# Kernel optimization log

Hardware: AMD Instinct MI355X
Metric: run time of the kernel (lower is better)

The kernel has to match this reference:

```python
import jax, jax.numpy as jnp
import numpy as np

K = 7          # kernel_size
STRIDE = 1
GC = 4         # group_channels (fixed in module)
BN_EPS = 1e-5


def setup_inputs() -> dict:
    key = jax.random.key(0)
    ks = jax.random.split(key, 4)
    B, C, H, W = 4, 256, 56, 56
    Cr = C // 4              # reduction_ratio = 4
    G = C // GC              # groups = 64
    K2 = K * K               # 49
    x = jax.random.normal(ks[0], (B, C, H, W), jnp.float32)
    w1 = jax.random.normal(ks[1], (Cr, C), jnp.float32) * 0.05   # conv1 1x1
    b1 = jnp.zeros((Cr,), jnp.float32)
    gamma = jnp.ones((Cr,), jnp.float32)
    beta = jnp.zeros((Cr,), jnp.float32)
    bn_mean = jnp.zeros((Cr,), jnp.float32)
    bn_var = jnp.ones((Cr,), jnp.float32)
    w2 = jax.random.normal(ks[2], (K2 * G, Cr), jnp.float32) * 0.05  # conv2 1x1
    b2 = jnp.zeros((K2 * G,), jnp.float32)
    return {"x": x, "w1": w1, "b1": b1, "gamma": gamma, "beta": beta,
            "bn_mean": bn_mean, "bn_var": bn_var, "w2": w2, "b2": b2}


def reference(x, w1, b1, gamma, beta, bn_mean, bn_var, w2, b2):
    B, C, H, W = x.shape
    G = C // GC
    K2 = K * K
    p = (K - 1) // 2

    # kernel-generation branch (stride == 1 -> no avgpool)
    y = jnp.einsum('oc,bchw->bohw', w1, x) + b1[None, :, None, None]
    # BatchNorm (inference, running stats)
    inv = gamma / jnp.sqrt(bn_var + BN_EPS)
    y = y * inv[None, :, None, None] + (beta - bn_mean * inv)[None, :, None, None]
    y = jax.nn.relu(y)
    weight = jnp.einsum('oc,bchw->bohw', w2, y) + b2[None, :, None, None]
    Ho, Wo = weight.shape[2], weight.shape[3]
    weight = weight.reshape(B, G, K2, Ho, Wo)

    # unfold: zero-pad then gather k*k shifted views (channel-major like torch Unfold)
    xp = jnp.pad(x, ((0, 0), (0, 0), (p, p), (p, p)))
    patches = jnp.stack(
        [xp[:, :, i:i + H:STRIDE, j:j + W:STRIDE] for i in range(K) for j in range(K)],
        axis=2)                                    # (B, C, K2, Ho, Wo)
    patches = patches.reshape(B, G, GC, K2, Ho, Wo)

    # per-pixel dynamic kernel multiply-accumulate over k^2
    out = jnp.einsum('bgkhw,bgckhw->bgchw', weight, patches)
    return out.reshape(B, C, Ho, Wo)
```

## Files before the change

### kernel.cpp

```cpp
#include <hip/hip_runtime.h>
#include <hip/hip_fp16.h>

typedef _Float16 h8 __attribute__((ext_vector_type(8)));
typedef _Float16 h2v __attribute__((ext_vector_type(2)));
typedef __fp16 fp16x2 __attribute__((ext_vector_type(2)));
typedef float f32x4 __attribute__((ext_vector_type(4)));

#define HW 3136
#define NPX 12544
#define YSTR 96
#define XROW 14
#define XSEG 148
#define PS2 456
#define WGT32_W 7296

union UH { unsigned int u; h2v h; fp16x2 p; };
__device__ __forceinline__ h2v uh(unsigned int u) { UH v; v.u = u; return v.h; }
__device__ __forceinline__ unsigned int hu(h2v h) { UH v; v.h = h; return v.u; }
#define BLO(w) __builtin_shufflevector(w, w, 0, 0)
#define BHI(w) __builtin_shufflevector(w, w, 1, 1)

__device__ __forceinline__ unsigned int pkrtz(float a, float b) {
    UH v; v.p = __builtin_amdgcn_cvt_pkrtz(a, b); return v.u;
}
__device__ __forceinline__ unsigned short f2hu(float f) {
    union { __half h; unsigned short u; } v; v.h = __float2half(f); return v.u;
}
__device__ __forceinline__ float fget(const float4& v, int e) {
    return e == 0 ? v.x : e == 1 ? v.y : e == 2 ? v.z : v.w;
}

__global__ __launch_bounds__(256) void kyw(
    const float* __restrict__ x, const float* __restrict__ w1,
    const float* __restrict__ b1, const float* __restrict__ gamma,
    const float* __restrict__ beta, const float* __restrict__ mean,
    const float* __restrict__ var, const float* __restrict__ w2,
    const float* __restrict__ b2, unsigned short* __restrict__ ytb,
    unsigned short* __restrict__ w2b96)
{
    __shared__ unsigned short xt[64 * 264];
    const int t = threadIdx.x, bid = blockIdx.x;

    if (bid >= 196) {
        const int r0 = (bid - 196) * 16;
#pragma unroll
        for (int i = 0; i < 6; ++i) {
            int j = i * 256 + t;
            int row = r0 + j / 96, col = j - (j / 96) * 96;
            int c8 = row / 448, rem = row - c8 * 448;
            int g = rem / 56, s = rem - g * 56;
            int ki = s >> 3, kj = s & 7;
            float v = 0.f;
            if (kj < 7) {
                int o = (c8 * 8 + g) * 49 + ki * 7 + kj;
                v = col < 64 ? w2[o * 64 + col] : (col == 64 ? b2[o] : 0.f);
            }
            w2b96[row * 96 + col] = f2hu(v);
        }
        return;
    }

    const int px0 = bid * 64;
    const int b = px0 / HW;
    const int p0 = px0 - b * HW;

    {
        unsigned int* xw = (unsigned int*)xt;
#pragma unroll
        for (int s = 0; s < 4; ++s)
#pragma unroll
            for (int i = 0; i < 2; ++i) {
                int j = i * 256 + t;
                int cp2 = j >> 2, pq = j & 3;
                const float* s0 = x + (size_t)(b * 256 + cp2 * 2) * HW
                                    + p0 + s * 16 + pq * 4;
                float4 v0 = *(const float4*)(s0);
                float4 v1 = *(const float4*)(s0 + HW);
                int pxb = s * 16 + pq * 4;
                xw[(pxb + 0) * 132 + cp2] = pkrtz(v0.x, v1.x);
                xw[(pxb + 1) * 132 + cp2] = pkrtz(v0.y, v1.y);
                xw[(pxb + 2) * 132 + cp2] = pkrtz(v0.z, v1.z);
                xw[(pxb + 3) * 132 + cp2] = pkrtz(v0.w, v1.w);
            }
    }
    if (t < 64) {
        unsigned short* yr = ytb + (size_t)(px0 + t) * YSTR + 64;
        ushort4 one; one.x = 0x3C00u; one.y = 0; one.z = 0; one.w = 0;
        ushort4 z; z.x = 0; z.y = 0; z.z = 0; z.w = 0;
        *(ushort4*)(yr) = one;
#pragma unroll
        for (int q = 1; q < 8; ++q) *(ushort4*)(yr + q * 4) = z;
    }
    __syncthreads();

    const int lane = t & 63, wave = t >> 6;
    const int n = lane & 15, quad = lane >> 4;
    const int m0 = wave * 16;

    h8 A[8];
#pragma unroll
    for (int k = 0; k < 8; ++k) {
        const float* wrow = w1 + (m0 + n) * 256 + k * 32 + quad * 8;
        float4 wa = *(const float4*)(wrow);
        float4 wb = *(const float4*)(wrow + 4);
        union { uint4 u; h8 h; } Au;
        Au.u.x = pkrtz(wa.x, wa.y);
        Au.u.y = pkrtz(wa.z, wa.w);
        Au.u.z = pkrtz(wb.x, wb.y);
        Au.u.w = pkrtz(wb.z, wb.w);
        A[k] = Au.h;
    }
    float sc[4], sh[4];
#pragma unroll
    for (int r = 0; r < 4; ++r) {
        int m = m0 + quad * 4 + r;
        sc[r] = gamma[m] * rsqrtf(var[m] + 1e-5f);
        sh[r] = beta[m] - mean[m] * sc[r] + b1[m] * sc[r];
    }

#pragma unroll
    for (int s = 0; s < 4; ++s) {
        f32x4 acc = {0.f, 0.f, 0.f, 0.f};
#pragma unroll
        for (int k = 0; k < 8; ++k) {
            h8 bv = *(const h8*)(&xt[(s * 16 + n) * 264 + k * 32 + quad * 8]);
            acc = __builtin_amdgcn_mfma_f32_16x16x32_f16(A[k], bv, acc, 0, 0, 0);
        }
        uint2 pk;
        pk.x = pkrtz(fmaxf(acc[0] * sc[0] + sh[0], 0.f),
                     fmaxf(acc[1] * sc[1] + sh[1], 0.f));
        pk.y = pkrtz(fmaxf(acc[2] * sc[2] + sh[2], 0.f),
                     fmaxf(acc[3] * sc[3] + sh[3], 0.f));
        *(uint2*)(ytb + (size_t)(px0 + s * 16 + n) * YSTR + m0 + quad * 4) = pk;
    }
}

__global__ __launch_bounds__(256, 4) void kmain(
    const float* __restrict__ x, const unsigned short* __restrict__ w2b96,
    const unsigned short* __restrict__ ytb, float* __restrict__ out)
{
    __shared__ __align__(16) unsigned int smem_u[WGT32_W + 16 * XSEG];
    unsigned short* wgt16 = (unsigned short*)smem_u;
    unsigned int* xsb = smem_u + WGT32_W;

    const int t = threadIdx.x;
    const int pix = t & 15, sub = t >> 4;
    const int lane = t & 63, wave = t >> 6;
    const int bc = blockIdx.x;
    const int b = bc >> 3, c8 = bc & 7;
    const int w0 = blockIdx.y * 8, h0 = blockIdx.z * 4;
    const int ph = pix >> 3, pw = pix & 7;
    const int n = lane & 15, quad = lane >> 4;

    h8 bfa[3], bfb[3];
    {
        const int Pa = b * HW + (h0 + (n >> 3)) * 56 + w0 + (n & 7);
        const unsigned short* ya = ytb + (size_t)Pa * YSTR + quad * 8;
        bfa[0] = *(const h8*)(ya);
        bfa[1] = *(const h8*)(ya + 32);
        bfa[2] = *(const h8*)(ya + 64);
        const unsigned short* yb = ya + (size_t)112 * YSTR;
        bfb[0] = *(const h8*)(yb);
        bfb[1] = *(const h8*)(yb + 32);
        bfb[2] = *(const h8*)(yb + 64);
    }

    if (t < 160) {
        const int seg = t & 15, jr = t >> 4;
        const int jg = seg >> 1, jcp = seg & 1;
        const int hh = h0 + jr - 3;
        const bool rowok = (hh >= 0) && (hh < 56);
        const float* src = x + ((size_t)b * 256 + c8 * 32 + jg * 4 + jcp * 2) * HW + hh * 56;
        float4 va[2][4];
#pragma unroll
        for (int q = 0; q < 4; ++q) {
            int col0 = w0 - 4 + q * 4;
            bool ok = rowok && (col0 >= 0) && (col0 <= 52);
#pragma unroll
            for (int ci = 0; ci < 2; ++ci)
                va[ci][q] = ok ? *(const float4*)(src + ci * HW + col0)
                              : make_float4(0.f, 0.f, 0.f, 0.f);
        }
        unsigned int* dst = xsb + seg * XSEG + jr * XROW;
#pragma unroll
        for (int q = 0; q < 4; ++q)
#pragma unroll
            for (int e = 0; e < 4; ++e) {
                int c = q * 4 + e - 1;
                if (c >= 0 && c < 14)
                    dst[c] = pkrtz(fget(va[0][q], e), fget(va[1][q], e));
            }
    }

    {
        const int c0 = c8 * 448;
        for (int tile = wave; tile < 28; tile += 4) {
            const unsigned short* ap = w2b96 + (size_t)(c0 + tile * 16 + n) * 96 + quad * 8;
            h8 af0 = *(const h8*)(ap);
            h8 af1 = *(const h8*)(ap + 32);
            h8 af2 = *(const h8*)(ap + 64);
            f32x4 aca = {0.f, 0.f, 0.f, 0.f};
            aca = __builtin_amdgcn_mfma_f32_16x16x32_f16(af0, bfa[0], aca, 0, 0, 0);
            aca = __builtin_amdgcn_mfma_f32_16x16x32_f16(af1, bfa[1], aca, 0, 0, 0);
            aca = __builtin_amdgcn_mfma_f32_16x16x32_f16(af2, bfa[2], aca, 0, 0, 0);
            f32x4 acb = {0.f, 0.f, 0.f, 0.f};
            acb = __builtin_amdgcn_mfma_f32_16x16x32_f16(af0, bfb[0], acb, 0, 0, 0);
            acb = __builtin_amdgcn_mfma_f32_16x16x32_f16(af1, bfb[1], acb, 0, 0, 0);
            acb = __builtin_amdgcn_mfma_f32_16x16x32_f16(af2, bfb[2], acb, 0, 0, 0);
            uint2 pka, pkb;
            pka.x = pkrtz(aca[0], aca[1]);
            pka.y = pkrtz(aca[2], aca[3]);
            pkb.x = pkrtz(acb[0], acb[1]);
            pkb.y = pkrtz(acb[2], acb[3]);
            *(uint2*)(wgt16 + n * PS2 + tile * 16 + quad * 4) = pka;
            *(uint2*)(wgt16 + (16 + n) * PS2 + tile * 16 + quad * 4) = pkb;
        }
    }
    __syncthreads();

    const int g = sub & 7, cp = sub >> 3;
    const unsigned int* xrb = xsb + (g * 2 + cp) * XSEG + pw;
#pragma unroll
    for (int php = 0; php < 2; ++php) {
        const unsigned short* wr16 = wgt16 + (php * 16 + pix) * PS2 + g * 56;
        const unsigned int* xr = xrb + (php * 2 + ph) * XROW;
        h2v acA = {(_Float16)0.f, (_Float16)0.f};
        h2v acB = acA;
#pragma unroll
        for (int ki = 0; ki < 7; ++ki) {
            uint4 wq = *(const uint4*)(wr16 + ki * 8);
            const unsigned int* xrow = xr + ki * XROW;
            unsigned int xv[7];
#pragma unroll
            for (int j = 0; j < 7; ++j) xv[j] = xrow[j];
            h2v w01 = uh(wq.x), w23 = uh(wq.y), w45 = uh(wq.z), w6p = uh(wq.w);
            acA += BLO(w01) * uh(xv[0]);
            acB += BHI(w01) * uh(xv[1]);
            acA += BLO(w23) * uh(xv[2]);
            acB += BHI(w23) * uh(xv[3]);
            acA += BLO(w45) * uh(xv[4]);
            acB += BHI(w45) * uh(xv[5]);
            acA += BLO(w6p) * uh(xv[6]);
        }
        h2v acc2 = acA + acB;
        int h = h0 + php * 2 + ph;
        size_t ob = ((size_t)b * 256 + c8 * 32 + g * 4 + cp * 2) * HW + h * 56 + w0 + pw;
        out[ob] = (float)acc2[0];
        out[ob + HW] = (float)acc2[1];
    }
}

extern "C" void kernel_launch(void* const* d_in, const int* in_sizes, int n_in,
                              void* d_out, int out_size, void* d_ws, size_t ws_size,
                              hipStream_t stream) {
    const float* x     = (const float*)d_in[0];
    const float* w1    = (const float*)d_in[1];
    const float* b1    = (const float*)d_in[2];
    const float* gamma = (const float*)d_in[3];
    const float* beta  = (const float*)d_in[4];
    const float* mean  = (const float*)d_in[5];
    const float* var   = (const float*)d_in[6];
    const float* w2    = (const float*)d_in[7];
    const float* b2    = (const float*)d_in[8];
    float* out = (float*)d_out;

    unsigned short* ytb   = (unsigned short*)d_ws;
    unsigned short* w2b96 = ytb + (size_t)NPX * YSTR;
    hipLaunchKernelGGL(kyw, dim3(420), dim3(256), 0, stream,
                       x, w1, b1, gamma, beta, mean, var, w2, b2, ytb, w2b96);
    hipLaunchKernelGGL(kmain, dim3(32, 7, 14), dim3(256), 0, stream,
                       x, w2b96, ytb, out);
}
```

Baseline: 121.7 us.

## Halve LDS weight buffer by staging second pixel half in registers

The per-pixel dynamic weights for the second 16-pixel half are held in registers (7 packed uint2 per thread) rather than written to shared memory alongside the first half. The LDS weight region is halved and reused: the first half is consumed, then the buffer is overwritten with the second half between two extra barriers. This lowers LDS per block so that six blocks per CU can be resident (launch bounds raised from 4 to 6). In exchange it adds two __syncthreads and extra register pressure from the held values.

```diff
diff --git a/kernel.cpp b/kernel.cpp
--- a/kernel.cpp
+++ b/kernel.cpp
@@ -12,7 +12,7 @@
 #define XROW 14
 #define XSEG 148
 #define PS2 456
-#define WGT32_W 7296
+#define WGT_W 3648
 
 union UH { unsigned int u; h2v h; fp16x2 p; };
 __device__ __forceinline__ h2v uh(unsigned int u) { UH v; v.u = u; return v.h; }
@@ -135,13 +135,13 @@
     }
 }
 
-__global__ __launch_bounds__(256, 4) void kmain(
+__global__ __launch_bounds__(256, 6) void kmain(
     const float* __restrict__ x, const unsigned short* __restrict__ w2b96,
     const unsigned short* __restrict__ ytb, float* __restrict__ out)
 {
-    __shared__ __align__(16) unsigned int smem_u[WGT32_W + 16 * XSEG];
+    __shared__ __align__(16) unsigned int smem_u[WGT_W + 16 * XSEG];
     unsigned short* wgt16 = (unsigned short*)smem_u;
-    unsigned int* xsb = smem_u + WGT32_W;
+    unsigned int* xsb = smem_u + WGT_W;
 
     const int t = threadIdx.x;
     const int pix = t & 15, sub = t >> 4;
@@ -159,10 +159,10 @@
         bfa[0] = *(const h8*)(ya);
         bfa[1] = *(const h8*)(ya + 32);
         bfa[2] = *(const h8*)(ya + 64);
-        const unsigned short* yb = ya + (size_t)112 * YSTR;
-        bfb[0] = *(const h8*)(yb);
-        bfb[1] = *(const h8*)(yb + 32);
-        bfb[2] = *(const h8*)(yb + 64);
+        const unsigned short* yb2 = ya + (size_t)112 * YSTR;
+        bfb[0] = *(const h8*)(yb2);
+        bfb[1] = *(const h8*)(yb2 + 32);
+        bfb[2] = *(const h8*)(yb2 + 64);
     }
 
     if (t < 160) {
@@ -192,9 +192,12 @@
             }
     }
 
+    uint2 pkb[7];
     {
         const int c0 = c8 * 448;
-        for (int tile = wave; tile < 28; tile += 4) {
+#pragma unroll
+        for (int j = 0; j < 7; ++j) {
+            const int tile = wave + 4 * j;
             const unsigned short* ap = w2b96 + (size_t)(c0 + tile * 16 + n) * 96 + quad * 8;
             h8 af0 = *(const h8*)(ap);
             h8 af1 = *(const h8*)(ap + 32);
@@ -207,23 +210,22 @@
             acb = __builtin_amdgcn_mfma_f32_16x16x32_f16(af0, bfb[0], acb, 0, 0, 0);
             acb = __builtin_amdgcn_mfma_f32_16x16x32_f16(af1, bfb[1], acb, 0, 0, 0);
             acb = __builtin_amdgcn_mfma_f32_16x16x32_f16(af2, bfb[2], acb, 0, 0, 0);
-            uint2 pka, pkb;
+            uint2 pka;
             pka.x = pkrtz(aca[0], aca[1]);
             pka.y = pkrtz(aca[2], aca[3]);
-            pkb.x = pkrtz(acb[0], acb[1]);
-            pkb.y = pkrtz(acb[2], acb[3]);
+            pkb[j].x = pkrtz(acb[0], acb[1]);
+            pkb[j].y = pkrtz(acb[2], acb[3]);
             *(uint2*)(wgt16 + n * PS2 + tile * 16 + quad * 4) = pka;
-            *(uint2*)(wgt16 + (16 + n) * PS2 + tile * 16 + quad * 4) = pkb;
         }
     }
     __syncthreads();
 
     const int g = sub & 7, cp = sub >> 3;
     const unsigned int* xrb = xsb + (g * 2 + cp) * XSEG + pw;
-#pragma unroll
-    for (int php = 0; php < 2; ++php) {
-        const unsigned short* wr16 = wgt16 + (php * 16 + pix) * PS2 + g * 56;
-        const unsigned int* xr = xrb + (php * 2 + ph) * XROW;
+    const unsigned short* wr16 = wgt16 + pix * PS2 + g * 56;
+
+    {
+        const unsigned int* xr = xrb + ph * XROW;
         h2v acA = {(_Float16)0.f, (_Float16)0.f};
         h2v acB = acA;
 #pragma unroll
@@ -243,8 +245,45 @@
             acA += BLO(w6p) * uh(xv[6]);
         }
         h2v acc2 = acA + acB;
-        int h = h0 + php * 2 + ph;
-        size_t ob = ((size_t)b * 256 + c8 * 32 + g * 4 + cp * 2) * HW + h * 56 + w0 + pw;
+        size_t ob = ((size_t)b * 256 + c8 * 32 + g * 4 + cp * 2) * HW
+                  + (h0 + ph) * 56 + w0 + pw;
+        out[ob] = (float)acc2[0];
+        out[ob + HW] = (float)acc2[1];
+    }
+    __syncthreads();
+
+    {
+#pragma unroll
+        for (int j = 0; j < 7; ++j) {
+            const int tile = wave + 4 * j;
+            *(uint2*)(wgt16 + n * PS2 + tile * 16 + quad * 4) = pkb[j];
+        }
+    }
+    __syncthreads();
+
+    {
+        const unsigned int* xr = xrb + (2 + ph) * XROW;
+        h2v acA = {(_Float16)0.f, (_Float16)0.f};
+        h2v acB = acA;
+#pragma unroll
+        for (int ki = 0; ki < 7; ++ki) {
+            uint4 wq = *(const uint4*)(wr16 + ki * 8);
+            const unsigned int* xrow = xr + ki * XROW;
+            unsigned int xv[7];
+#pragma unroll
+            for (int j = 0; j < 7; ++j) xv[j] = xrow[j];
+            h2v w01 = uh(wq.x), w23 = uh(wq.y), w45 = uh(wq.z), w6p = uh(wq.w);
+            acA += BLO(w01) * uh(xv[0]);
+            acB += BHI(w01) * uh(xv[1]);
+            acA += BLO(w23) * uh(xv[2]);
+            acB += BHI(w23) * uh(xv[3]);
+            acA += BLO(w45) * uh(xv[4]);
+            acB += BHI(w45) * uh(xv[5]);
+            acA += BLO(w6p) * uh(xv[6]);
+        }
+        h2v acc2 = acA + acB;
+        size_t ob = ((size_t)b * 256 + c8 * 32 + g * 4 + cp * 2) * HW
+                  + (h0 + 2 + ph) * 56 + w0 + pw;
         out[ob] = (float)acc2[0];
         out[ob + HW] = (float)acc2[1];
     }
```

Measured after the change: 118.6 us. 1.03x faster.
